# Kernel optimization log

Measured on AMD Instinct MI355X. Metric: run time of the kernel, lower is better.

The kernel has to match this reference:

```python
import jax, jax.numpy as jnp
import numpy as np
import math

B, S, D, H = 1, 2048, 4096, 32
HD = D // H  # 128
BASE = 10000.0
NEG = -1e9


def rotate_half(x):
    x1, x2 = x[..., : x.shape[-1] // 2], x[..., x.shape[-1] // 2 :]
    return jnp.concatenate((-x2, x1), axis=-1)


def setup_inputs() -> dict:
    key = jax.random.key(0)
    ks = jax.random.split(key, 5)
    scale = 1.0 / math.sqrt(D)
    hidden_states = jax.random.normal(ks[0], (B, S, D), dtype=jnp.float32)
    Wq = jax.random.normal(ks[1], (D, D), dtype=jnp.float32) * scale
    Wk = jax.random.normal(ks[2], (D, D), dtype=jnp.float32) * scale
    Wv = jax.random.normal(ks[3], (D, D), dtype=jnp.float32) * scale
    Wo = jax.random.normal(ks[4], (D, D), dtype=jnp.float32) * scale
    # causal additive mask [1,1,S,S]
    causal = jnp.tril(jnp.ones((S, S), dtype=bool))
    attention_mask = jnp.where(causal, 0.0, NEG).astype(jnp.float32)[None, None]
    # rotary cos/sin cache [1,1,S,HD]
    inv_freq = 1.0 / (BASE ** (jnp.arange(0, HD, 2, dtype=jnp.float32) / HD))
    freqs = jnp.arange(S, dtype=jnp.float32)[:, None] * inv_freq[None, :]
    emb = jnp.concatenate((freqs, freqs), axis=-1)
    cos = jnp.cos(emb)[None, None]
    sin = jnp.sin(emb)[None, None]
    return dict(hidden_states=hidden_states, attention_mask=attention_mask,
                cos=cos, sin=sin, Wq=Wq, Wk=Wk, Wv=Wv, Wo=Wo)


def reference(hidden_states, attention_mask, cos, sin, Wq, Wk, Wv, Wo):
    b, s, d = hidden_states.shape
    # projections (torch Linear: x @ W.T), reshape to [B,H,S,HD]
    def proj(W):
        return (hidden_states @ W.T).reshape(b, s, H, HD).transpose(0, 2, 1, 3)
    q, k, v = proj(Wq), proj(Wk), proj(Wv)
    # RoPE
    q = q * cos + rotate_half(q) * sin
    k = k * cos + rotate_half(k) * sin
    # scores [B,H,S,S], key pre-scaled as in original
    scores = jnp.einsum('bhqd,bhkd->bhqk', q, k / math.sqrt(HD)) + attention_mask
    attn = jax.nn.softmax(scores.astype(jnp.float32), axis=-1).astype(scores.dtype)
    out = jnp.einsum('bhqk,bhkd->bhqd', attn, v)
    out = out.transpose(0, 2, 1, 3).reshape(b, s, d)
    return out @ Wo.T
```

## Files before the change

### kernel.cpp

```cpp
#include <hip/hip_runtime.h>
#include <hip/hip_bf16.h>
#include <stdint.h>

#define DEV __device__ __forceinline__

typedef __bf16 bf16x8 __attribute__((ext_vector_type(8)));
typedef float f32x4 __attribute__((ext_vector_type(4)));
typedef unsigned short ushort8_t __attribute__((ext_vector_type(8)));
typedef unsigned short ushort4_t __attribute__((ext_vector_type(4)));

constexpr int S = 2048;
constexpr int D = 4096;
constexpr int H = 32;
constexpr int HD = 128;
constexpr float kSc = 0.08838834764831845f * 1.4426950408889634f;

DEV unsigned short f2bf(float f) {
    uint32_t u = __builtin_bit_cast(uint32_t, f);
    u += 0x7fffu + ((u >> 16) & 1u);
    return (unsigned short)(u >> 16);
}
DEV float bf2f(unsigned short h) {
    uint32_t u = ((uint32_t)h) << 16;
    return __builtin_bit_cast(float, u);
}

DEV void gload_lds16(const void* g, void* l) {
    __builtin_amdgcn_global_load_lds(
        (const __attribute__((address_space(1))) void*)g,
        (__attribute__((address_space(3))) void*)l,
        16, 0, 0);
}

DEV f32x4 mfma16(bf16x8 a, bf16x8 b, f32x4 c) {
    return __builtin_amdgcn_mfma_f32_16x16x32_bf16(a, b, c, 0, 0, 0);
}

__global__ __launch_bounds__(256) void cvt_all(const float* __restrict__ hs,
                                               const float* __restrict__ w0,
                                               const float* __restrict__ w1,
                                               const float* __restrict__ w2,
                                               const float* __restrict__ w3,
                                               unsigned short* __restrict__ hsb,
                                               unsigned short* __restrict__ o0,
                                               unsigned short* __restrict__ o1,
                                               unsigned short* __restrict__ o2,
                                               unsigned short* __restrict__ o3) {
    const int b = blockIdx.x;
    const float* in;
    unsigned short* out;
    size_t blk;
    if (b < 4096) {
        in = hs; out = hsb; blk = (size_t)b;
    } else {
        const int i = b - 4096;
        const int w = i >> 13;
        const int r = i & 8191;
        in  = (w == 0) ? w0 : (w == 1) ? w1 : (w == 2) ? w2 : w3;
        out = (w == 0) ? o0 : (w == 1) ? o1 : (w == 2) ? o2 : o3;
        blk = (size_t)r;
    }
    const size_t i8 = blk * 256 + threadIdx.x;
    f32x4 a = ((const f32x4*)in)[2 * i8];
    f32x4 c = ((const f32x4*)in)[2 * i8 + 1];
    ushort8_t o;
    o[0] = f2bf(a[0]); o[1] = f2bf(a[1]); o[2] = f2bf(a[2]); o[3] = f2bf(a[3]);
    o[4] = f2bf(c[0]); o[5] = f2bf(c[1]); o[6] = f2bf(c[2]); o[7] = f2bf(c[3]);
    ((ushort8_t*)out)[i8] = o;
}

__global__ __launch_bounds__(256) void gemm_qkv(const unsigned short* __restrict__ A,
                                                const unsigned short* __restrict__ wq,
                                                const unsigned short* __restrict__ wk,
                                                const unsigned short* __restrict__ wv,
                                                unsigned short* __restrict__ Qb,
                                                unsigned short* __restrict__ Kb,
                                                unsigned short* __restrict__ Vt) {
    __shared__ unsigned short As[128 * 64];
    __shared__ unsigned short Bs[128 * 64];
    const int t = threadIdx.x;
    const int lane = t & 63;
    const int wid = t >> 6;
    const int g = lane >> 4;
    const int rl = lane & 15;

    const int bid = blockIdx.x;
    const int wg = (bid & 7) * 192 + (bid >> 3);
    const int xx = wg % 96;
    const int yy = wg / 96;
    const int m0 = yy * 128;
    const int n0g = xx * 128;
    const int wsel = n0g >> 12;
    const int n0 = n0g & 4095;
    const unsigned short* B = (wsel == 0) ? wq : (wsel == 1) ? wk : wv;

    const int wm = (wid >> 1) * 64;
    const int wn = (wid & 1) * 64;
    constexpr int K = D, M = S, N = D;

    f32x4 acc[4][4] = {};

    for (int kt = 0; kt < K; kt += 64) {
#pragma unroll
        for (int r = 0; r < 4; ++r) {
            const int c = r * 256 + t;
            const int row = c >> 3;
            const int src = (c & 7) ^ (row & 7);
            const int dstChunk = r * 256 + wid * 64;
            gload_lds16(A + (size_t)(m0 + row) * K + kt + src * 8, &As[dstChunk * 8]);
            gload_lds16(B + (size_t)(n0 + row) * K + kt + src * 8, &Bs[dstChunk * 8]);
        }
        __syncthreads();
#pragma unroll
        for (int ks = 0; ks < 2; ++ks) {
            bf16x8 af[4], bfv[4];
#pragma unroll
            for (int i = 0; i < 4; ++i) {
                const int rowa = wm + i * 16 + rl;
                af[i] = *(const bf16x8*)&As[rowa * 64 + (((ks * 4 + g) ^ (rowa & 7)) << 3)];
                const int rowb = wn + i * 16 + rl;
                bfv[i] = *(const bf16x8*)&Bs[rowb * 64 + (((ks * 4 + g) ^ (rowb & 7)) << 3)];
            }
#pragma unroll
            for (int mi = 0; mi < 4; ++mi)
#pragma unroll
                for (int ni = 0; ni < 4; ++ni)
                    acc[mi][ni] = mfma16(af[mi], bfv[ni], acc[mi][ni]);
        }
        __syncthreads();
    }

#pragma unroll
    for (int mi = 0; mi < 4; ++mi) {
#pragma unroll
        for (int ni = 0; ni < 4; ++ni) {
            const int grow = m0 + wm + mi * 16 + g * 4;
            const int gcol = n0 + wn + ni * 16 + rl;
            if (wsel == 2) {
                ushort4_t v;
#pragma unroll
                for (int r = 0; r < 4; ++r) v[r] = f2bf(acc[mi][ni][r]);
                *(ushort4_t*)&Vt[(size_t)gcol * M + grow] = v;
            } else {
                unsigned short* o = (wsel == 0) ? Qb : Kb;
#pragma unroll
                for (int r = 0; r < 4; ++r)
                    o[(size_t)(grow + r) * N + gcol] = f2bf(acc[mi][ni][r]);
            }
        }
    }
}

__global__ __launch_bounds__(256) void gemm_out(const unsigned short* __restrict__ A,
                                                const unsigned short* __restrict__ B,
                                                float* __restrict__ C) {
    __shared__ unsigned short As[128 * 64];
    __shared__ unsigned short Bs[128 * 64];
    const int t = threadIdx.x;
    const int lane = t & 63;
    const int wid = t >> 6;
    const int g = lane >> 4;
    const int rl = lane & 15;

    const int bid = blockIdx.x;
    const int wg = (bid & 7) * 64 + (bid >> 3);
    const int xx = wg % 32;
    const int yy = wg / 32;
    const int m0 = yy * 128;
    const int n0 = xx * 128;

    const int wm = (wid >> 1) * 64;
    const int wn = (wid & 1) * 64;
    constexpr int K = D, N = D;

    f32x4 acc[4][4] = {};

    for (int kt = 0; kt < K; kt += 64) {
#pragma unroll
        for (int r = 0; r < 4; ++r) {
            const int c = r * 256 + t;
            const int row = c >> 3;
            const int src = (c & 7) ^ (row & 7);
            const int dstChunk = r * 256 + wid * 64;
            gload_lds16(A + (size_t)(m0 + row) * K + kt + src * 8, &As[dstChunk * 8]);
            gload_lds16(B + (size_t)(n0 + row) * K + kt + src * 8, &Bs[dstChunk * 8]);
        }
        __syncthreads();
#pragma unroll
        for (int ks = 0; ks < 2; ++ks) {
            bf16x8 af[4], bfv[4];
#pragma unroll
            for (int i = 0; i < 4; ++i) {
                const int rowa = wm + i * 16 + rl;
                af[i] = *(const bf16x8*)&As[rowa * 64 + (((ks * 4 + g) ^ (rowa & 7)) << 3)];
                const int rowb = wn + i * 16 + rl;
                bfv[i] = *(const bf16x8*)&Bs[rowb * 64 + (((ks * 4 + g) ^ (rowb & 7)) << 3)];
            }
#pragma unroll
            for (int mi = 0; mi < 4; ++mi)
#pragma unroll
                for (int ni = 0; ni < 4; ++ni)
                    acc[mi][ni] = mfma16(af[mi], bfv[ni], acc[mi][ni]);
        }
        __syncthreads();
    }

#pragma unroll
    for (int mi = 0; mi < 4; ++mi) {
#pragma unroll
        for (int ni = 0; ni < 4; ++ni) {
            const int grow = m0 + wm + mi * 16 + g * 4;
            const int gcol = n0 + wn + ni * 16 + rl;
#pragma unroll
            for (int r = 0; r < 4; ++r)
                C[(size_t)(grow + r) * N + gcol] = acc[mi][ni][r];
        }
    }
}

__global__ __launch_bounds__(256) void rope_kernel(unsigned short* __restrict__ Qb,
                                                   unsigned short* __restrict__ Kb,
                                                   const float* __restrict__ cosT,
                                                   const float* __restrict__ sinT) {
    const int i = blockIdx.x * 256 + threadIdx.x;
    const int j8 = i & 7;
    const int h = (i >> 3) & 31;
    const int s = i >> 8;
    const size_t base = (size_t)s * D + h * HD + j8 * 8;
    const float* cp = cosT + s * HD + j8 * 8;
    const float* sp = sinT + s * HD + j8 * 8;
    float c1[8], s1[8], c2[8], s2[8];
#pragma unroll
    for (int k = 0; k < 8; ++k) { c1[k] = cp[k]; s1[k] = sp[k]; c2[k] = cp[k + 64]; s2[k] = sp[k + 64]; }

#pragma unroll
    for (int w = 0; w < 2; ++w) {
        unsigned short* p = (w == 0 ? Qb : Kb) + base;
        const float f = (w == 0) ? kSc : 1.0f;
        ushort8_t x1 = *(ushort8_t*)p;
        ushort8_t x2 = *(ushort8_t*)(p + 64);
        ushort8_t o1, o2;
#pragma unroll
        for (int k = 0; k < 8; ++k) {
            const float a = bf2f(x1[k]);
            const float b = bf2f(x2[k]);
            o1[k] = f2bf((a * c1[k] - b * s1[k]) * f);
            o2[k] = f2bf((b * c2[k] + a * s2[k]) * f);
        }
        *(ushort8_t*)p = o1;
        *(ushort8_t*)(p + 64) = o2;
    }
}

constexpr int NQT = S / 128;
__global__ __launch_bounds__(256, 2) void flash_attn(const unsigned short* __restrict__ Q,
                                                     const unsigned short* __restrict__ K,
                                                     const unsigned short* __restrict__ V,
                                                     unsigned short* __restrict__ O) {
    __shared__ unsigned short Ks[2][64 * 128];
    __shared__ unsigned short Vs[128 * 64];
    __shared__ unsigned short Ps[4][32 * 64];

    const int t = threadIdx.x;
    const int lane = t & 63;
    const int wid = t >> 6;
    const int g = lane >> 4;
    const int rl = lane & 15;
    const int bid = blockIdx.x;
    const int qt = (NQT - 1) - (bid >> 5);
    const int h = bid & 31;
    const int q0 = qt * 128;
    const int wrow0 = q0 + wid * 32;

    bf16x8 qf[2][4];
#pragma unroll
    for (int mi = 0; mi < 2; ++mi) {
        const unsigned short* qp = Q + (size_t)(wrow0 + mi * 16 + rl) * D + h * HD;
#pragma unroll
        for (int ks = 0; ks < 4; ++ks) qf[mi][ks] = *(const bf16x8*)(qp + ks * 32 + g * 8);
    }

    f32x4 accO[2][8] = {};
    float m2s[2] = {-1e30f, -1e30f};
    float lsum[2] = {0.f, 0.f};

#pragma unroll
    for (int r = 0; r < 4; ++r) {
        const int c = r * 256 + t;
        const int rowk = c >> 4;
        const int srck = (c & 15) ^ (rowk & 7);
        gload_lds16(K + (size_t)rowk * D + h * HD + srck * 8,
                    &Ks[0][(r * 256 + wid * 64) * 8]);
    }
    __syncthreads();

    int cur = 0;
    const int ntiles = 2 * qt + 2;
    for (int kv = 0; kv < ntiles; ++kv) {
        const int kv0 = kv * 64;
#pragma unroll
        for (int r = 0; r < 4; ++r) {
            const int c = r * 256 + t;
            const int rowv = c >> 3;
            const int srcv = (c & 7) ^ (rowv & 7);
            gload_lds16(V + (size_t)(h * HD + rowv) * S + kv0 + srcv * 8,
                        &Vs[(r * 256 + wid * 64) * 8]);
        }
        if (kv + 1 < ntiles) {
#pragma unroll
            for (int r = 0; r < 4; ++r) {
                const int c = r * 256 + t;
                const int rowk = c >> 4;
                const int srck = (c & 15) ^ (rowk & 7);
                gload_lds16(K + (size_t)(kv0 + 64 + rowk) * D + h * HD + srck * 8,
                            &Ks[cur ^ 1][(r * 256 + wid * 64) * 8]);
            }
        }

        const bool active = kv0 <= wrow0 + 31;
        if (active) {
            f32x4 sf[2][4];
#pragma unroll
            for (int mi = 0; mi < 2; ++mi)
#pragma unroll
                for (int nt = 0; nt < 4; ++nt) sf[mi][nt] = f32x4{0.f, 0.f, 0.f, 0.f};
            __builtin_amdgcn_s_setprio(1);
#pragma unroll
            for (int nt = 0; nt < 4; ++nt) {
                const int row = nt * 16 + rl;
#pragma unroll
                for (int ks = 0; ks < 4; ++ks) {
                    bf16x8 kf = *(const bf16x8*)&Ks[cur][row * 128 + (((ks * 4 + g) ^ (row & 7)) << 3)];
                    sf[0][nt] = mfma16(kf, qf[0][ks], sf[0][nt]);
                    sf[1][nt] = mfma16(kf, qf[1][ks], sf[1][nt]);
                }
            }
            __builtin_amdgcn_s_setprio(0);

            const bool needMask = (kv0 + 63 > wrow0);
            float cf2[2];
            bool chg = false;
#pragma unroll
            for (int mi = 0; mi < 2; ++mi) {
                const int qrow = wrow0 + mi * 16 + rl;
                float mx = -1e30f;
                if (needMask) {
#pragma unroll
                    for (int nt = 0; nt < 4; ++nt)
#pragma unroll
                        for (int r = 0; r < 4; ++r) {
                            const int kcol = kv0 + nt * 16 + g * 4 + r;
                            float s = sf[mi][nt][r];
                            s = (kcol > qrow) ? -1e30f : s;
                            sf[mi][nt][r] = s;
                            mx = fmaxf(mx, s);
                        }
                } else {
#pragma unroll
                    for (int nt = 0; nt < 4; ++nt)
#pragma unroll
                        for (int r = 0; r < 4; ++r) mx = fmaxf(mx, sf[mi][nt][r]);
                }
                mx = fmaxf(mx, __shfl_xor(mx, 16));
                mx = fmaxf(mx, __shfl_xor(mx, 32));
                const float mn = fmaxf(m2s[mi], mx);
                cf2[mi] = __builtin_amdgcn_exp2f(m2s[mi] - mn);
                chg |= (mn > m2s[mi]);
                m2s[mi] = mn;
                float rs = 0.f;
#pragma unroll
                for (int nt = 0; nt < 4; ++nt)
#pragma unroll
                    for (int r = 0; r < 4; ++r) {
                        const float p = __builtin_amdgcn_exp2f(sf[mi][nt][r] - mn);
                        sf[mi][nt][r] = p;
                        rs += p;
                    }
                rs += __shfl_xor(rs, 16);
                rs += __shfl_xor(rs, 32);
                lsum[mi] = lsum[mi] * cf2[mi] + rs;
            }

            if (__any((int)chg)) {
#pragma unroll
                for (int mi = 0; mi < 2; ++mi)
#pragma unroll
                    for (int nt = 0; nt < 8; ++nt)
#pragma unroll
                        for (int r = 0; r < 4; ++r) accO[mi][nt][r] *= cf2[mi];
            }

            unsigned short* myP = Ps[wid];
#pragma unroll
            for (int mi = 0; mi < 2; ++mi) {
                const int row = mi * 16 + rl;
                const int rx = row & 7;
#pragma unroll
                for (int nt = 0; nt < 4; ++nt) {
                    ushort4_t v;
#pragma unroll
                    for (int r = 0; r < 4; ++r) v[r] = f2bf(sf[mi][nt][r]);
                    const int chunk = nt * 2 + (g >> 1);
                    *(ushort4_t*)&myP[row * 64 + ((chunk ^ rx) << 3) + ((g & 1) << 2)] = v;
                }
            }
        }
        __syncthreads();

        if (active) {
            unsigned short* myP = Ps[wid];
            __builtin_amdgcn_s_setprio(1);
#pragma unroll
            for (int ks = 0; ks < 2; ++ks) {
                bf16x8 pa[2];
#pragma unroll
                for (int mi = 0; mi < 2; ++mi) {
                    const int row = mi * 16 + rl;
                    pa[mi] = *(const bf16x8*)&myP[row * 64 + (((ks * 4 + g) ^ (row & 7)) << 3)];
                }
#pragma unroll
                for (int nt = 0; nt < 8; ++nt) {
                    const int vrow = nt * 16 + rl;
                    bf16x8 vf = *(const bf16x8*)&Vs[vrow * 64 + (((ks * 4 + g) ^ (vrow & 7)) << 3)];
                    accO[0][nt] = mfma16(vf, pa[0], accO[0][nt]);
                    accO[1][nt] = mfma16(vf, pa[1], accO[1][nt]);
                }
            }
            __builtin_amdgcn_s_setprio(0);
        }
        __syncthreads();
        cur ^= 1;
    }

#pragma unroll
    for (int mi = 0; mi < 2; ++mi) {
        const float inv = 1.0f / lsum[mi];
        const int qrow = wrow0 + mi * 16 + rl;
#pragma unroll
        for (int nt = 0; nt < 8; ++nt) {
            ushort4_t v;
#pragma unroll
            for (int r = 0; r < 4; ++r) v[r] = f2bf(accO[mi][nt][r] * inv);
            *(ushort4_t*)&O[(size_t)qrow * D + h * HD + nt * 16 + g * 4] = v;
        }
    }
}

extern "C" void kernel_launch(void* const* d_in, const int* in_sizes, int n_in,
                              void* d_out, int out_size, void* d_ws, size_t ws_size,
                              hipStream_t stream) {
    const float* hs   = (const float*)d_in[0];
    const float* cosT = (const float*)d_in[2];
    const float* sinT = (const float*)d_in[3];
    const float* Wq   = (const float*)d_in[4];
    const float* Wk   = (const float*)d_in[5];
    const float* Wv   = (const float*)d_in[6];
    const float* Wo   = (const float*)d_in[7];

    char* ws = (char*)d_ws;
    const size_t MB = 1ull << 20;
    unsigned short* hsb = (unsigned short*)(ws);
    unsigned short* wqb = (unsigned short*)(ws + 16 * MB);
    unsigned short* wkb = (unsigned short*)(ws + 48 * MB);
    unsigned short* wvb = (unsigned short*)(ws + 80 * MB);
    unsigned short* wob = (unsigned short*)(ws + 112 * MB);
    unsigned short* Qb  = (unsigned short*)(ws + 144 * MB);
    unsigned short* Kb  = (unsigned short*)(ws + 160 * MB);
    unsigned short* Vt  = (unsigned short*)(ws + 176 * MB);
    unsigned short* AOb = (unsigned short*)(ws + 192 * MB);

    cvt_all<<<4096 + 4 * 8192, 256, 0, stream>>>(hs, Wq, Wk, Wv, Wo,
                                                 hsb, wqb, wkb, wvb, wob);

    gemm_qkv<<<1536, 256, 0, stream>>>(hsb, wqb, wkb, wvb, Qb, Kb, Vt);

    rope_kernel<<<2048, 256, 0, stream>>>(Qb, Kb, cosT, sinT);

    flash_attn<<<dim3(NQT * H), 256, 0, stream>>>(Qb, Kb, Vt, AOb);

    gemm_out<<<512, 256, 0, stream>>>(AOb, wob, (float*)d_out);
}
```

Baseline: 498.1 us.

## Rewrite QKV GEMM as 256x256-tile, 8-wave, multi-buffered pipelined kernel

Replaces the 128x128 single-stage QKV projection GEMM with a 256x256 tile kernel using 512 threads, 128 KB of dynamic LDS holding four A and four B half-tile buffers, and a phased schedule. Global-to-LDS loads for upcoming k-steps are issued inside each compute phase, with explicit vmcnt waits, barriers and s_setprio around the MFMA bursts. The goal is to overlap memory traffic with matrix math and raise data reuse per loaded tile. The cost is much higher register and LDS pressure, one block per CU at most, and fragile hand-written synchronisation.

```diff
diff --git a/kernel.cpp b/kernel.cpp
--- a/kernel.cpp
+++ b/kernel.cpp
@@ -69,86 +69,136 @@
     ((ushort8_t*)out)[i8] = o;
 }
 
-__global__ __launch_bounds__(256) void gemm_qkv(const unsigned short* __restrict__ A,
-                                                const unsigned short* __restrict__ wq,
-                                                const unsigned short* __restrict__ wk,
-                                                const unsigned short* __restrict__ wv,
-                                                unsigned short* __restrict__ Qb,
-                                                unsigned short* __restrict__ Kb,
-                                                unsigned short* __restrict__ Vt) {
-    __shared__ unsigned short As[128 * 64];
-    __shared__ unsigned short Bs[128 * 64];
-    const int t = threadIdx.x;
-    const int lane = t & 63;
-    const int wid = t >> 6;
-    const int g = lane >> 4;
+__global__ __launch_bounds__(512, 2) void gemm_qkv8(const unsigned short* __restrict__ Ap,
+                                                    const unsigned short* __restrict__ wq,
+                                                    const unsigned short* __restrict__ wk,
+                                                    const unsigned short* __restrict__ wv,
+                                                    unsigned short* __restrict__ Qb,
+                                                    unsigned short* __restrict__ Kb,
+                                                    unsigned short* __restrict__ Vt) {
+    extern __shared__ unsigned short lds8[];
+    unsigned short (*As)[8192] = (unsigned short(*)[8192])lds8;
+    unsigned short (*Bs)[8192] = (unsigned short(*)[8192])(lds8 + 32768);
+
+    const int tix = threadIdx.x;
+    const int lane = tix & 63;
+    const int w = tix >> 6;
+    const int g = (lane >> 4);
     const int rl = lane & 15;
+    const int wm = w >> 2;
+    const int wn = w & 3;
+    const int bh = wn >> 1;
+    const int bc0 = (wn & 1) * 64;
 
     const int bid = blockIdx.x;
-    const int wg = (bid & 7) * 192 + (bid >> 3);
-    const int xx = wg % 96;
-    const int yy = wg / 96;
-    const int m0 = yy * 128;
-    const int n0g = xx * 128;
+    const int wg = (bid & 7) * 48 + (bid >> 3);
+    const int xx = wg % 48;
+    const int yy = wg / 48;
+    const int m0 = yy * 256;
+    const int n0g = xx * 256;
     const int wsel = n0g >> 12;
     const int n0 = n0g & 4095;
-    const unsigned short* B = (wsel == 0) ? wq : (wsel == 1) ? wk : wv;
-
-    const int wm = (wid >> 1) * 64;
-    const int wn = (wid & 1) * 64;
-    constexpr int K = D, M = S, N = D;
-
-    f32x4 acc[4][4] = {};
-
-    for (int kt = 0; kt < K; kt += 64) {
-#pragma unroll
-        for (int r = 0; r < 4; ++r) {
-            const int c = r * 256 + t;
-            const int row = c >> 3;
-            const int src = (c & 7) ^ (row & 7);
-            const int dstChunk = r * 256 + wid * 64;
-            gload_lds16(A + (size_t)(m0 + row) * K + kt + src * 8, &As[dstChunk * 8]);
-            gload_lds16(B + (size_t)(n0 + row) * K + kt + src * 8, &Bs[dstChunk * 8]);
-        }
-        __syncthreads();
-#pragma unroll
-        for (int ks = 0; ks < 2; ++ks) {
-            bf16x8 af[4], bfv[4];
-#pragma unroll
-            for (int i = 0; i < 4; ++i) {
-                const int rowa = wm + i * 16 + rl;
-                af[i] = *(const bf16x8*)&As[rowa * 64 + (((ks * 4 + g) ^ (rowa & 7)) << 3)];
-                const int rowb = wn + i * 16 + rl;
-                bfv[i] = *(const bf16x8*)&Bs[rowb * 64 + (((ks * 4 + g) ^ (rowb & 7)) << 3)];
-            }
-#pragma unroll
-            for (int mi = 0; mi < 4; ++mi)
-#pragma unroll
-                for (int ni = 0; ni < 4; ++ni)
-                    acc[mi][ni] = mfma16(af[mi], bfv[ni], acc[mi][ni]);
-        }
-        __syncthreads();
-    }
-
-#pragma unroll
-    for (int mi = 0; mi < 4; ++mi) {
-#pragma unroll
-        for (int ni = 0; ni < 4; ++ni) {
-            const int grow = m0 + wm + mi * 16 + g * 4;
-            const int gcol = n0 + wn + ni * 16 + rl;
-            if (wsel == 2) {
-                ushort4_t v;
-#pragma unroll
-                for (int r = 0; r < 4; ++r) v[r] = f2bf(acc[mi][ni][r]);
-                *(ushort4_t*)&Vt[(size_t)gcol * M + grow] = v;
-            } else {
-                unsigned short* o = (wsel == 0) ? Qb : Kb;
-#pragma unroll
-                for (int r = 0; r < 4; ++r)
-                    o[(size_t)(grow + r) * N + gcol] = f2bf(acc[mi][ni][r]);
-            }
-        }
-    }
+    const unsigned short* Bp = (wsel == 0) ? wq : (wsel == 1) ? wk : wv;
+
+    int srow[2], scol[2];
+#pragma unroll
+    for (int u = 0; u < 2; ++u) {
+        const int d = (u * 512 + tix) * 16;
+        const int sby = d ^ (((d >> 9) & 1) << 5);
+        srow[u] = sby >> 7;
+        scol[u] = (sby & 127) >> 1;
+    }
+
+    const char* aBase[2] = {(const char*)As[wm], (const char*)As[2 + wm]};
+    const char* bBase[2] = {(const char*)Bs[bh], (const char*)Bs[2 + bh]};
+
+    f32x4 acc[4][2][4] = {};
+    bf16x8 bfr[4][2];
+
+#define STG_A(kt, h, slot)                                                        \
+    if ((kt) < 64) {                                                              \
+        _Pragma("unroll") for (int u = 0; u < 2; ++u)                             \
+            gload_lds16(Ap + (size_t)(m0 + (h) * 128 + srow[u]) * 4096 +          \
+                            (kt) * 64 + scol[u],                                  \
+                        &As[slot][(u * 512 + tix) * 8]);                          \
+    }
+#define STG_B(kt, h, slot)                                                        \
+    if ((kt) < 64) {                                                              \
+        _Pragma("unroll") for (int u = 0; u < 2; ++u)                             \
+            gload_lds16(Bp + (size_t)(n0 + (h) * 128 + srow[u]) * 4096 +          \
+                            (kt) * 64 + scol[u],                                  \
+                        &Bs[slot][(u * 512 + tix) * 8]);                          \
+    }
+
+#define PHASE(pt, q, STG, VM)                                                     \
+    {                                                                             \
+        bf16x8 af[2][2];                                                          \
+        _Pragma("unroll") for (int mi = 0; mi < 2; ++mi)                          \
+        _Pragma("unroll") for (int ks = 0; ks < 2; ++ks) {                        \
+            int ab = ((q) * 32 + mi * 16 + rl) * 128 + ks * 64 + g * 16;          \
+            ab ^= ((ab >> 9) & 1) << 5;                                           \
+            af[mi][ks] = *(const bf16x8*)(aBase[pt] + ab);                        \
+        }                                                                         \
+        if ((q) == 0) {                                                           \
+            _Pragma("unroll") for (int nt = 0; nt < 4; ++nt)                      \
+            _Pragma("unroll") for (int ks = 0; ks < 2; ++ks) {                    \
+                int bb = (bc0 + nt * 16 + rl) * 128 + ks * 64 + g * 16;           \
+                bb ^= ((bb >> 9) & 1) << 5;                                       \
+                bfr[nt][ks] = *(const bf16x8*)(bBase[pt] + bb);                   \
+            }                                                                     \
+        }                                                                         \
+        STG;                                                                      \
+        if (VM) asm volatile("s_waitcnt vmcnt(4)" ::: "memory");                  \
+        __builtin_amdgcn_s_barrier();                                             \
+        __builtin_amdgcn_s_setprio(1);                                            \
+        _Pragma("unroll") for (int ks = 0; ks < 2; ++ks)                          \
+        _Pragma("unroll") for (int mi = 0; mi < 2; ++mi)                          \
+        _Pragma("unroll") for (int nt = 0; nt < 4; ++nt)                          \
+            acc[q][mi][nt] = mfma16(af[mi][ks], bfr[nt][ks], acc[q][mi][nt]);     \
+        __builtin_amdgcn_s_setprio(0);                                            \
+        __builtin_amdgcn_s_barrier();                                             \
+    }
+
+    STG_A(0, 0, 0); STG_A(0, 1, 1);
+    STG_B(0, 0, 0); STG_B(0, 1, 1);
+    STG_B(1, 0, 2); STG_B(1, 1, 3);
+    __syncthreads();
+
+    for (int i = 0; i < 32; ++i) {
+        const int o = 2 * i + 1, ne = 2 * i + 2, no = 2 * i + 3;
+        PHASE(0, 0, STG_A(o, 0, 2), 0)
+        PHASE(0, 1, STG_A(o, 1, 3), 0)
+        PHASE(0, 2, STG_B(ne, 0, 0), 0)
+        PHASE(0, 3, STG_B(ne, 1, 1), 1)
+        PHASE(1, 0, STG_A(ne, 0, 0), 0)
+        PHASE(1, 1, STG_A(ne, 1, 1), 0)
+        PHASE(1, 2, STG_B(no, 0, 2), 0)
+        PHASE(1, 3, STG_B(no, 1, 3), 1)
+    }
+#undef PHASE
+#undef STG_A
+#undef STG_B
+
+#pragma unroll
+    for (int q = 0; q < 4; ++q)
+#pragma unroll
+        for (int mi = 0; mi < 2; ++mi)
+#pragma unroll
+            for (int nt = 0; nt < 4; ++nt) {
+                const int row0 = m0 + wm * 128 + q * 32 + mi * 16 + g * 4;
+                const int colg = n0 + wn * 64 + nt * 16 + rl;
+                if (wsel == 2) {
+                    ushort4_t v;
+#pragma unroll
+                    for (int r = 0; r < 4; ++r) v[r] = f2bf(acc[q][mi][nt][r]);
+                    *(ushort4_t*)&Vt[(size_t)colg * S + row0] = v;
+                } else {
+                    unsigned short* o = (wsel == 0) ? Qb : Kb;
+#pragma unroll
+                    for (int r = 0; r < 4; ++r)
+                        o[(size_t)(row0 + r) * 4096 + colg] = f2bf(acc[q][mi][nt][r]);
+                }
+            }
 }
 
 __global__ __launch_bounds__(256) void gemm_out(const unsigned short* __restrict__ A,
@@ -472,7 +522,7 @@
     cvt_all<<<4096 + 4 * 8192, 256, 0, stream>>>(hs, Wq, Wk, Wv, Wo,
                                                  hsb, wqb, wkb, wvb, wob);
 
-    gemm_qkv<<<1536, 256, 0, stream>>>(hsb, wqb, wkb, wvb, Qb, Kb, Vt);
+    gemm_qkv8<<<384, 512, 131072, stream>>>(hsb, wqb, wkb, wvb, Qb, Kb, Vt);
 
     rope_kernel<<<2048, 256, 0, stream>>>(Qb, Kb, cosT, sinT);
 
```

Measured after the change: 484.4 us. 2.7% less time.
